# Optimization experiments

Hardware: AMD Instinct MI355X
Metric: run time of the kernel (lower is better)

Reference implementation:

```python
import jax, jax.numpy as jnp
import numpy as np

OUT, IN, GS = 16384, 4096, 16
G = OUT * IN // GS  # 4194304 groups


def setup_inputs() -> dict:
    key = jax.random.key(0)
    k1, k2, k3, k4 = jax.random.split(key, 4)
    x = jax.random.normal(k1, (8, 32, IN), dtype=jnp.float32)
    weight_q2 = jax.random.randint(k2, (G, GS // 4), 0, 256, dtype=jnp.int32)
    weight_norm = jax.random.uniform(k3, (G, 1), dtype=jnp.float16)
    bias = jax.random.normal(k4, (OUT,), dtype=jnp.float32)
    return {"x": x, "weight_q2": weight_q2, "weight_norm": weight_norm, "bias": bias}


def _dequant_2bit(weight_q2, weight_norm):
    # torch: xq_out[:, i::4] = (xq >> 2i) & 3  =>  element index within group = i + 4*k
    # where k = packed column (slow, stride 4), i = shift index (fast).
    norm = weight_norm.astype(jnp.float32)                      # [G, 1]
    shifts = jnp.arange(4, dtype=jnp.int32) * 2                 # [4]
    vals = (weight_q2[:, :, None] >> shifts) & 3                # [G, 4(pack k), 4(shift i)]
    xq_out = vals.astype(jnp.float32).reshape(G, GS)            # [G, 16], layout k*4 + i
    w = (xq_out / 3.0) * (2.0 * norm) - norm                    # [G, 16]
    return w.reshape(OUT, IN)


def reference(x, weight_q2, weight_norm, bias):
    w = _dequant_2bit(weight_q2, weight_norm)                   # [OUT, IN] fp32
    return jnp.einsum('bsi,oi->bso', x, w) + bias
```

## Files before the change

kernel.cpp:

```cpp
#include <hip/hip_runtime.h>
#include <stdint.h>

#define M_DIM 256
#define N_DIM 16384
#define K_DIM 4096
#define BN 64
#define BK 64
#define NT (K_DIM / BK)

typedef __bf16 bf16x8 __attribute__((ext_vector_type(8)));
typedef float  f32x4  __attribute__((ext_vector_type(4)));

__device__ __forceinline__ uint32_t f2bf(float f) {
  uint32_t u = __float_as_uint(f);
  return (u + 0x7fffu + ((u >> 16) & 1u)) >> 16;
}

#define LDS_BARRIER() \
  asm volatile("s_waitcnt lgkmcnt(0)\n\ts_barrier" ::: "memory")

__global__ __launch_bounds__(256) void cvt_x_kernel(const float* __restrict__ x,
                                                    uint4* __restrict__ ws) {
  int T = blockIdx.x * 256 + threadIdx.x;
  int mb_glob = T >> 13;
  int r       = T & 8191;
  int kch     = r >> 6;
  int L       = r & 63;
  int row = mb_glob * 16 + (L & 15);
  int k   = kch * 32 + (L >> 4) * 8;
  const float* p = x + (size_t)row * K_DIM + k;
  float4 a = *(const float4*)p;
  float4 b = *(const float4*)(p + 4);
  uint4 o;
  o.x = f2bf(a.x) | (f2bf(a.y) << 16);
  o.y = f2bf(a.z) | (f2bf(a.w) << 16);
  o.z = f2bf(b.x) | (f2bf(b.y) << 16);
  o.w = f2bf(b.z) | (f2bf(b.w) << 16);
  ws[T] = o;
}

__device__ __forceinline__ uint4 deq8(uint32_t qx, uint32_t qy, uint32_t tlo,
                                      uint32_t thi) {
  uint32_t s0 = ((qx & 3u) | ((qx & 0xCu) << 14)) * 0x0202u + 0x01000100u;
  uint32_t s1 = (((qx >> 4) & 3u) | ((qx & 0xC0u) << 10)) * 0x0202u + 0x01000100u;
  uint32_t s2 = ((qy & 3u) | ((qy & 0xCu) << 14)) * 0x0202u + 0x01000100u;
  uint32_t s3 = (((qy >> 4) & 3u) | ((qy & 0xC0u) << 10)) * 0x0202u + 0x01000100u;
  uint4 r;
  r.x = __builtin_amdgcn_perm(thi, tlo, s0);
  r.y = __builtin_amdgcn_perm(thi, tlo, s1);
  r.z = __builtin_amdgcn_perm(thi, tlo, s2);
  r.w = __builtin_amdgcn_perm(thi, tlo, s3);
  return r;
}

__global__ __launch_bounds__(512, 4) void gemm2bit_kernel(
    const uint4*    __restrict__ aws,
    const uint32_t* __restrict__ q2,
    const float*    __restrict__ nrm,
    const float*    __restrict__ bias,
    float*          __restrict__ out)
{
  __shared__ uint4 Bb[2][512];

  const int tid  = threadIdx.x;
  const int lane = tid & 63;
  const int w    = tid >> 6;
  const int lo4  = lane & 15;
  const int qd   = lane >> 4;
  const int n0   = blockIdx.x * BN;
  const int m0   = blockIdx.y * 128;

  if (w < 4) {
    const int cw  = w;
    const int lrs = lane ^ qd;

    const uint4* pA = aws + (size_t)(blockIdx.y * 8 + cw * 2) * 8192 + lane;

    f32x4 acc[2][4];
#pragma unroll
    for (int s = 0; s < 2; ++s)
#pragma unroll
      for (int u = 0; u < 4; ++u)
        acc[s][u] = (f32x4){0.f, 0.f, 0.f, 0.f};

    uint4 afE[4], afO[4];
#pragma unroll
    for (int s = 0; s < 2; ++s)
#pragma unroll
      for (int ts = 0; ts < 2; ++ts)
        afE[s * 2 + ts] = pA[(size_t)s * 8192 + ts * 64];
    LDS_BARRIER();

#define CONS_BODY(T, PR, AFC, AFN)                                              \
    do {                                                                        \
      if ((T) + 1 < NT) {                                                       \
        size_t toff = (size_t)((T) + 1) * 128;                                  \
        _Pragma("unroll")                                                       \
        for (int s = 0; s < 2; ++s)                                             \
          _Pragma("unroll")                                                     \
          for (int ts = 0; ts < 2; ++ts)                                        \
            AFN[s * 2 + ts] = pA[(size_t)s * 8192 + toff + ts * 64];            \
      }                                                                         \
      __builtin_amdgcn_s_setprio(1);                                            \
      _Pragma("unroll")                                                         \
      for (int ts = 0; ts < 2; ++ts) {                                          \
        bf16x8 bfv[4];                                                          \
        _Pragma("unroll")                                                       \
        for (int u = 0; u < 4; ++u)                                             \
          bfv[u] = *(const bf16x8*)&Bb[PR][(ts * 4 + u) * 64 + lrs];            \
        _Pragma("unroll")                                                       \
        for (int s = 0; s < 2; ++s) {                                           \
          bf16x8 av = __builtin_bit_cast(bf16x8, AFC[s * 2 + ts]);              \
          _Pragma("unroll")                                                     \
          for (int u = 0; u < 4; ++u)                                           \
            acc[s][u] = __builtin_amdgcn_mfma_f32_16x16x32_bf16(av, bfv[u],     \
                                                            acc[s][u], 0, 0, 0);\
        }                                                                       \
      }                                                                         \
      __builtin_amdgcn_s_setprio(0);                                            \
      LDS_BARRIER();                                                            \
    } while (0)

    for (int t2 = 0; t2 < NT; t2 += 2) {
      CONS_BODY(t2,     0, afE, afO);
      CONS_BODY(t2 + 1, 1, afO, afE);
    }
#undef CONS_BODY

    float bv[4];
#pragma unroll
    for (int u = 0; u < 4; ++u)
      bv[u] = bias[n0 + u * 16 + lo4];
#pragma unroll
    for (int s = 0; s < 2; ++s) {
      int mrow = m0 + cw * 32 + s * 16 + qd * 4;
#pragma unroll
      for (int u = 0; u < 4; ++u) {
        int ncol = n0 + u * 16 + lo4;
        float* p = out + (size_t)mrow * N_DIM + ncol;
#pragma unroll
        for (int r = 0; r < 4; ++r)
          p[(size_t)r * N_DIM] = acc[s][u][r] + bv[u];
      }
    }
  } else {
    const int pw    = w - 4;
    const int kg    = lane & 3;
    const int n_loc = lane >> 2;
    const int grow  = n0 + pw * 16 + n_loc;
    const int qd2a  = (kg & 1) * 2;
    const int qd2b  = qd2a + 1;
    const int bsA = ((kg >> 1) * 4 + pw) * 64 + qd2a * 16 + (n_loc ^ qd2a);
    const int bsB = ((kg >> 1) * 4 + pw) * 64 + qd2b * 16 + (n_loc ^ qd2b);

    const uint32_t* pq = q2 + ((size_t)grow * 256 + kg) * 4;
    const float*    pn = nrm + (size_t)grow * 256 + kg;

    uint4 q0 = *(const uint4*)pq;
    float y0 = pn[0];
    uint4 qE = *(const uint4*)(pq + 16);
    float nE = pn[4];
    uint4 qO = *(const uint4*)(pq + 32);
    float nO = pn[8];
    {
      float a2 = y0 * (2.0f / 3.0f);
      uint32_t tlo = f2bf(-y0) | (f2bf(fmaf(1.0f, a2, -y0)) << 16);
      uint32_t thi = f2bf(fmaf(2.0f, a2, -y0)) | (f2bf(fmaf(3.0f, a2, -y0)) << 16);
      Bb[0][bsA] = deq8(q0.x, q0.y, tlo, thi);
      Bb[0][bsB] = deq8(q0.z, q0.w, tlo, thi);
    }
    LDS_BARRIER();

#define PROD_BODY(T, PR, QQ, NN)                                                \
    do {                                                                        \
      if ((T) + 1 < NT) {                                                       \
        float a2 = NN * (2.0f / 3.0f);                                          \
        uint32_t tlo = f2bf(-NN) | (f2bf(fmaf(1.0f, a2, -NN)) << 16);           \
        uint32_t thi = f2bf(fmaf(2.0f, a2, -NN)) |                              \
                       (f2bf(fmaf(3.0f, a2, -NN)) << 16);                       \
        Bb[(PR) ^ 1][bsA] = deq8(QQ.x, QQ.y, tlo, thi);                         \
        Bb[(PR) ^ 1][bsB] = deq8(QQ.z, QQ.w, tlo, thi);                         \
      }                                                                         \
      if ((T) + 3 < NT) {                                                       \
        QQ = *(const uint4*)(pq + (size_t)((T) + 3) * 16);                      \
        NN = pn[(size_t)((T) + 3) * 4];                                         \
      }                                                                         \
      LDS_BARRIER();                                                            \
    } while (0)

    for (int t2 = 0; t2 < NT; t2 += 2) {
      PROD_BODY(t2,     0, qE, nE);
      PROD_BODY(t2 + 1, 1, qO, nO);
    }
#undef PROD_BODY
  }
}

extern "C" void kernel_launch(void* const* d_in, const int* in_sizes, int n_in,
                              void* d_out, int out_size, void* d_ws, size_t ws_size,
                              hipStream_t stream) {
  const float*    x    = (const float*)d_in[0];
  const uint32_t* q2   = (const uint32_t*)d_in[1];
  const float*    nm   = (const float*)d_in[2];
  const float*    bias = (const float*)d_in[3];
  float*          out  = (float*)d_out;
  uint4*          aws  = (uint4*)d_ws;

  cvt_x_kernel<<<512, 256, 0, stream>>>(x, aws);
  gemm2bit_kernel<<<dim3(N_DIM / BN, 2), 512, 0, stream>>>(aws, q2, nm, bias, out);
}
```

Baseline: 153.9 us.

## Deepen LDS ring to four stages and retile consumer warps 2x2

The shared B buffer grows from two to four stages, so producer warps dequantize two K-tiles per barrier and the barrier count is halved. Consumer warps are remapped from a 4x1 to a 2x2 layout, each computing 64 rows by 32 columns. Each consumer now reads two B fragments from LDS per step instead of four, and keeps four A fragments in flight. The cost is twice the LDS footprint and more A registers per warp, which may reduce occupancy.

```diff
diff --git a/kernel.cpp b/kernel.cpp
--- a/kernel.cpp
+++ b/kernel.cpp
@@ -60,7 +60,7 @@
     const float*    __restrict__ bias,
     float*          __restrict__ out)
 {
-  __shared__ uint4 Bb[2][512];
+  __shared__ uint4 Bb[4][512];
 
   const int tid  = threadIdx.x;
   const int lane = tid & 63;
@@ -71,72 +71,71 @@
   const int m0   = blockIdx.y * 128;
 
   if (w < 4) {
-    const int cw  = w;
+    const int wm  = w >> 1;
+    const int wn  = w & 1;
     const int lrs = lane ^ qd;
 
-    const uint4* pA = aws + (size_t)(blockIdx.y * 8 + cw * 2) * 8192 + lane;
-
-    f32x4 acc[2][4];
-#pragma unroll
-    for (int s = 0; s < 2; ++s)
-#pragma unroll
-      for (int u = 0; u < 4; ++u)
+    const uint4* pA = aws + (size_t)(blockIdx.y * 8 + wm * 4) * 8192 + lane;
+
+    f32x4 acc[4][2];
+#pragma unroll
+    for (int s = 0; s < 4; ++s)
+#pragma unroll
+      for (int u = 0; u < 2; ++u)
         acc[s][u] = (f32x4){0.f, 0.f, 0.f, 0.f};
 
     uint4 afE[4], afO[4];
 #pragma unroll
-    for (int s = 0; s < 2; ++s)
-#pragma unroll
-      for (int ts = 0; ts < 2; ++ts)
-        afE[s * 2 + ts] = pA[(size_t)s * 8192 + ts * 64];
+    for (int s = 0; s < 4; ++s) afE[s] = pA[(size_t)s * 8192];
+    const uint4* pAp = pA + 64;
+    int cnext = 1;
     LDS_BARRIER();
 
-#define CONS_BODY(T, PR, AFC, AFN)                                              \
+#define CONS_STEP(BUF, TS, AFC, AFN)                                            \
     do {                                                                        \
-      if ((T) + 1 < NT) {                                                       \
-        size_t toff = (size_t)((T) + 1) * 128;                                  \
+      if (cnext < 128) {                                                        \
         _Pragma("unroll")                                                       \
-        for (int s = 0; s < 2; ++s)                                             \
-          _Pragma("unroll")                                                     \
-          for (int ts = 0; ts < 2; ++ts)                                        \
-            AFN[s * 2 + ts] = pA[(size_t)s * 8192 + toff + ts * 64];            \
+        for (int s = 0; s < 4; ++s) AFN[s] = pAp[(size_t)s * 8192];             \
       }                                                                         \
+      pAp += 64; ++cnext;                                                       \
       __builtin_amdgcn_s_setprio(1);                                            \
+      bf16x8 bv0 = *(const bf16x8*)&Bb[BUF][((TS) * 4 + wn * 2) * 64 + lrs];    \
+      bf16x8 bv1 = *(const bf16x8*)&Bb[BUF][((TS) * 4 + wn * 2 + 1) * 64 + lrs];\
       _Pragma("unroll")                                                         \
-      for (int ts = 0; ts < 2; ++ts) {                                          \
-        bf16x8 bfv[4];                                                          \
-        _Pragma("unroll")                                                       \
-        for (int u = 0; u < 4; ++u)                                             \
-          bfv[u] = *(const bf16x8*)&Bb[PR][(ts * 4 + u) * 64 + lrs];            \
-        _Pragma("unroll")                                                       \
-        for (int s = 0; s < 2; ++s) {                                           \
-          bf16x8 av = __builtin_bit_cast(bf16x8, AFC[s * 2 + ts]);              \
-          _Pragma("unroll")                                                     \
-          for (int u = 0; u < 4; ++u)                                           \
-            acc[s][u] = __builtin_amdgcn_mfma_f32_16x16x32_bf16(av, bfv[u],     \
-                                                            acc[s][u], 0, 0, 0);\
-        }                                                                       \
+      for (int s = 0; s < 4; ++s) {                                             \
+        bf16x8 av = __builtin_bit_cast(bf16x8, AFC[s]);                         \
+        acc[s][0] = __builtin_amdgcn_mfma_f32_16x16x32_bf16(av, bv0,            \
+                                                            acc[s][0], 0, 0, 0);\
+        acc[s][1] = __builtin_amdgcn_mfma_f32_16x16x32_bf16(av, bv1,            \
+                                                            acc[s][1], 0, 0, 0);\
       }                                                                         \
       __builtin_amdgcn_s_setprio(0);                                            \
-      LDS_BARRIER();                                                            \
     } while (0)
 
-    for (int t2 = 0; t2 < NT; t2 += 2) {
-      CONS_BODY(t2,     0, afE, afO);
-      CONS_BODY(t2 + 1, 1, afO, afE);
-    }
-#undef CONS_BODY
-
-    float bv[4];
-#pragma unroll
-    for (int u = 0; u < 4; ++u)
-      bv[u] = bias[n0 + u * 16 + lo4];
-#pragma unroll
-    for (int s = 0; s < 2; ++s) {
-      int mrow = m0 + cw * 32 + s * 16 + qd * 4;
-#pragma unroll
-      for (int u = 0; u < 4; ++u) {
-        int ncol = n0 + u * 16 + lo4;
+    for (int tp = 0; tp < NT; tp += 4) {
+      CONS_STEP(0, 0, afE, afO);
+      CONS_STEP(0, 1, afO, afE);
+      CONS_STEP(1, 0, afE, afO);
+      CONS_STEP(1, 1, afO, afE);
+      LDS_BARRIER();
+      CONS_STEP(2, 0, afE, afO);
+      CONS_STEP(2, 1, afO, afE);
+      CONS_STEP(3, 0, afE, afO);
+      CONS_STEP(3, 1, afO, afE);
+      LDS_BARRIER();
+    }
+#undef CONS_STEP
+
+    float bv[2];
+#pragma unroll
+    for (int u = 0; u < 2; ++u)
+      bv[u] = bias[n0 + wn * 32 + u * 16 + lo4];
+#pragma unroll
+    for (int s = 0; s < 4; ++s) {
+      int mrow = m0 + wm * 64 + s * 16 + qd * 4;
+#pragma unroll
+      for (int u = 0; u < 2; ++u) {
+        int ncol = n0 + wn * 32 + u * 16 + lo4;
         float* p = out + (size_t)mrow * N_DIM + ncol;
 #pragma unroll
         for (int r = 0; r < 4; ++r)
@@ -156,43 +155,53 @@
     const uint32_t* pq = q2 + ((size_t)grow * 256 + kg) * 4;
     const float*    pn = nrm + (size_t)grow * 256 + kg;
 
-    uint4 q0 = *(const uint4*)pq;
-    float y0 = pn[0];
-    uint4 qE = *(const uint4*)(pq + 16);
-    float nE = pn[4];
-    uint4 qO = *(const uint4*)(pq + 32);
-    float nO = pn[8];
+#define DEQ_TILE(WB, Q, NV)                                                     \
+    do {                                                                        \
+      float a2_ = (NV) * (2.0f / 3.0f);                                         \
+      uint32_t tlo_ = f2bf(-(NV)) | (f2bf(fmaf(1.0f, a2_, -(NV))) << 16);       \
+      uint32_t thi_ = f2bf(fmaf(2.0f, a2_, -(NV))) |                            \
+                      (f2bf(fmaf(3.0f, a2_, -(NV))) << 16);                     \
+      Bb[WB][bsA] = deq8((Q).x, (Q).y, tlo_, thi_);                             \
+      Bb[WB][bsB] = deq8((Q).z, (Q).w, tlo_, thi_);                             \
+    } while (0)
+
     {
-      float a2 = y0 * (2.0f / 3.0f);
-      uint32_t tlo = f2bf(-y0) | (f2bf(fmaf(1.0f, a2, -y0)) << 16);
-      uint32_t thi = f2bf(fmaf(2.0f, a2, -y0)) | (f2bf(fmaf(3.0f, a2, -y0)) << 16);
-      Bb[0][bsA] = deq8(q0.x, q0.y, tlo, thi);
-      Bb[0][bsB] = deq8(q0.z, q0.w, tlo, thi);
-    }
+      uint4 t0 = *(const uint4*)pq;         float y0 = pn[0];
+      uint4 t1 = *(const uint4*)(pq + 16);  float y1 = pn[4];
+      DEQ_TILE(0, t0, y0);
+      DEQ_TILE(1, t1, y1);
+    }
+    uint4 qE0 = *(const uint4*)(pq + 32);  float nE0 = pn[8];
+    uint4 qE1 = *(const uint4*)(pq + 48);  float nE1 = pn[12];
+    uint4 qO0 = *(const uint4*)(pq + 64);  float nO0 = pn[16];
+    uint4 qO1 = *(const uint4*)(pq + 80);  float nO1 = pn[20];
+    const uint32_t* pql = pq + 96;
+    const float*    pnl = pn + 24;
     LDS_BARRIER();
 
-#define PROD_BODY(T, PR, QQ, NN)                                                \
-    do {                                                                        \
-      if ((T) + 1 < NT) {                                                       \
-        float a2 = NN * (2.0f / 3.0f);                                          \
-        uint32_t tlo = f2bf(-NN) | (f2bf(fmaf(1.0f, a2, -NN)) << 16);           \
-        uint32_t thi = f2bf(fmaf(2.0f, a2, -NN)) |                              \
-                       (f2bf(fmaf(3.0f, a2, -NN)) << 16);                       \
-        Bb[(PR) ^ 1][bsA] = deq8(QQ.x, QQ.y, tlo, thi);                         \
-        Bb[(PR) ^ 1][bsB] = deq8(QQ.z, QQ.w, tlo, thi);                         \
-      }                                                                         \
-      if ((T) + 3 < NT) {                                                       \
-        QQ = *(const uint4*)(pq + (size_t)((T) + 3) * 16);                      \
-        NN = pn[(size_t)((T) + 3) * 4];                                         \
-      }                                                                         \
-      LDS_BARRIER();                                                            \
-    } while (0)
-
-    for (int t2 = 0; t2 < NT; t2 += 2) {
-      PROD_BODY(t2,     0, qE, nE);
-      PROD_BODY(t2 + 1, 1, qO, nO);
-    }
-#undef PROD_BODY
+    for (int tp = 0; tp < NT; tp += 4) {
+      if (tp + 2 < NT) {
+        DEQ_TILE(2, qE0, nE0);
+        DEQ_TILE(3, qE1, nE1);
+      }
+      if (tp + 6 < NT) {
+        qE0 = *(const uint4*)pql;        nE0 = pnl[0];
+        qE1 = *(const uint4*)(pql + 16); nE1 = pnl[4];
+      }
+      pql += 32; pnl += 8;
+      LDS_BARRIER();
+      if (tp + 4 < NT) {
+        DEQ_TILE(0, qO0, nO0);
+        DEQ_TILE(1, qO1, nO1);
+      }
+      if (tp + 8 < NT) {
+        qO0 = *(const uint4*)pql;        nO0 = pnl[0];
+        qO1 = *(const uint4*)(pql + 16); nO1 = pnl[4];
+      }
+      pql += 32; pnl += 8;
+      LDS_BARRIER();
+    }
+#undef DEQ_TILE
   }
 }
 
```

Result: slower. 161.1 us (+4.7%).

## Halve block M-tile to 64 rows with two consumer and two producer waves

Applied to the files above, without the earlier changes.

Shrinks each workgroup from 512 to 256 threads: two consumer waves cover 64 M rows and two producer waves each dequantize two weight rows per step. The grid doubles in the M dimension to 4 to keep coverage the same. This gives finer scheduling granularity and more blocks per CU, but the full weight matrix is now loaded and dequantized four times instead of twice, which doubles the producer-side global traffic and ALU work.

```diff
diff --git a/kernel.cpp b/kernel.cpp
--- a/kernel.cpp
+++ b/kernel.cpp
@@ -53,7 +53,7 @@
   return r;
 }
 
-__global__ __launch_bounds__(512, 4) void gemm2bit_kernel(
+__global__ __launch_bounds__(256) void gemm2bit_kernel(
     const uint4*    __restrict__ aws,
     const uint32_t* __restrict__ q2,
     const float*    __restrict__ nrm,
@@ -68,13 +68,13 @@
   const int lo4  = lane & 15;
   const int qd   = lane >> 4;
   const int n0   = blockIdx.x * BN;
-  const int m0   = blockIdx.y * 128;
-
-  if (w < 4) {
+  const int m0   = blockIdx.y * 64;
+
+  if (w < 2) {
     const int cw  = w;
     const int lrs = lane ^ qd;
 
-    const uint4* pA = aws + (size_t)(blockIdx.y * 8 + cw * 2) * 8192 + lane;
+    const uint4* pA = aws + (size_t)(blockIdx.y * 4 + cw * 2) * 8192 + lane;
 
     f32x4 acc[2][4];
 #pragma unroll
@@ -144,55 +144,70 @@
       }
     }
   } else {
-    const int pw    = w - 4;
+    const int p     = w - 2;
     const int kg    = lane & 3;
     const int n_loc = lane >> 2;
-    const int grow  = n0 + pw * 16 + n_loc;
+    const int ra    = n0 + p * 32 + n_loc;
+    const int rb    = ra + 16;
+    const int nba   = p * 2;
+    const int nbb   = p * 2 + 1;
     const int qd2a  = (kg & 1) * 2;
     const int qd2b  = qd2a + 1;
-    const int bsA = ((kg >> 1) * 4 + pw) * 64 + qd2a * 16 + (n_loc ^ qd2a);
-    const int bsB = ((kg >> 1) * 4 + pw) * 64 + qd2b * 16 + (n_loc ^ qd2b);
-
-    const uint32_t* pq = q2 + ((size_t)grow * 256 + kg) * 4;
-    const float*    pn = nrm + (size_t)grow * 256 + kg;
-
-    uint4 q0 = *(const uint4*)pq;
-    float y0 = pn[0];
-    uint4 qE = *(const uint4*)(pq + 16);
-    float nE = pn[4];
-    uint4 qO = *(const uint4*)(pq + 32);
-    float nO = pn[8];
+    const int ba    = ((kg >> 1) * 4 + nba) * 64;
+    const int bb    = ((kg >> 1) * 4 + nbb) * 64;
+    const int sAa = ba + qd2a * 16 + (n_loc ^ qd2a);
+    const int sBa = ba + qd2b * 16 + (n_loc ^ qd2b);
+    const int sAb = bb + qd2a * 16 + (n_loc ^ qd2a);
+    const int sBb = bb + qd2b * 16 + (n_loc ^ qd2b);
+
+    const uint32_t* pqa = q2 + ((size_t)ra * 256 + kg) * 4;
+    const uint32_t* pqb = q2 + ((size_t)rb * 256 + kg) * 4;
+    const float*    pna = nrm + (size_t)ra * 256 + kg;
+    const float*    pnb = nrm + (size_t)rb * 256 + kg;
+
+#define DEQ_GROUP(WB, Q, NV, SA, SB)                                            \
+    do {                                                                        \
+      float a2_ = (NV) * (2.0f / 3.0f);                                         \
+      uint32_t tlo_ = f2bf(-(NV)) | (f2bf(fmaf(1.0f, a2_, -(NV))) << 16);       \
+      uint32_t thi_ = f2bf(fmaf(2.0f, a2_, -(NV))) |                            \
+                      (f2bf(fmaf(3.0f, a2_, -(NV))) << 16);                     \
+      Bb[WB][SA] = deq8((Q).x, (Q).y, tlo_, thi_);                              \
+      Bb[WB][SB] = deq8((Q).z, (Q).w, tlo_, thi_);                              \
+    } while (0)
+
     {
-      float a2 = y0 * (2.0f / 3.0f);
-      uint32_t tlo = f2bf(-y0) | (f2bf(fmaf(1.0f, a2, -y0)) << 16);
-      uint32_t thi = f2bf(fmaf(2.0f, a2, -y0)) | (f2bf(fmaf(3.0f, a2, -y0)) << 16);
-      Bb[0][bsA] = deq8(q0.x, q0.y, tlo, thi);
-      Bb[0][bsB] = deq8(q0.z, q0.w, tlo, thi);
-    }
+      uint4 t0a = *(const uint4*)pqa;  float y0a = pna[0];
+      uint4 t0b = *(const uint4*)pqb;  float y0b = pnb[0];
+      DEQ_GROUP(0, t0a, y0a, sAa, sBa);
+      DEQ_GROUP(0, t0b, y0b, sAb, sBb);
+    }
+    uint4 qEa = *(const uint4*)(pqa + 16);  float nEa = pna[4];
+    uint4 qEb = *(const uint4*)(pqb + 16);  float nEb = pnb[4];
+    uint4 qOa = *(const uint4*)(pqa + 32);  float nOa = pna[8];
+    uint4 qOb = *(const uint4*)(pqb + 32);  float nOb = pnb[8];
     LDS_BARRIER();
 
-#define PROD_BODY(T, PR, QQ, NN)                                                \
+#define PROD_BODY(T, PR, QA, NA, QB, NB)                                        \
     do {                                                                        \
       if ((T) + 1 < NT) {                                                       \
-        float a2 = NN * (2.0f / 3.0f);                                          \
-        uint32_t tlo = f2bf(-NN) | (f2bf(fmaf(1.0f, a2, -NN)) << 16);           \
-        uint32_t thi = f2bf(fmaf(2.0f, a2, -NN)) |                              \
-                       (f2bf(fmaf(3.0f, a2, -NN)) << 16);                       \
-        Bb[(PR) ^ 1][bsA] = deq8(QQ.x, QQ.y, tlo, thi);                         \
-        Bb[(PR) ^ 1][bsB] = deq8(QQ.z, QQ.w, tlo, thi);                         \
+        DEQ_GROUP((PR) ^ 1, QA, NA, sAa, sBa);                                  \
+        DEQ_GROUP((PR) ^ 1, QB, NB, sAb, sBb);                                  \
       }                                                                         \
       if ((T) + 3 < NT) {                                                       \
-        QQ = *(const uint4*)(pq + (size_t)((T) + 3) * 16);                      \
-        NN = pn[(size_t)((T) + 3) * 4];                                         \
+        QA = *(const uint4*)(pqa + (size_t)((T) + 3) * 16);                     \
+        NA = pna[(size_t)((T) + 3) * 4];                                        \
+        QB = *(const uint4*)(pqb + (size_t)((T) + 3) * 16);                     \
+        NB = pnb[(size_t)((T) + 3) * 4];                                        \
       }                                                                         \
       LDS_BARRIER();                                                            \
     } while (0)
 
     for (int t2 = 0; t2 < NT; t2 += 2) {
-      PROD_BODY(t2,     0, qE, nE);
-      PROD_BODY(t2 + 1, 1, qO, nO);
+      PROD_BODY(t2,     0, qEa, nEa, qEb, nEb);
+      PROD_BODY(t2 + 1, 1, qOa, nOa, qOb, nOb);
     }
 #undef PROD_BODY
+#undef DEQ_GROUP
   }
 }
 
@@ -207,5 +222,5 @@
   uint4*          aws  = (uint4*)d_ws;
 
   cvt_x_kernel<<<512, 256, 0, stream>>>(x, aws);
-  gemm2bit_kernel<<<dim3(N_DIM / BN, 2), 512, 0, stream>>>(aws, q2, nm, bias, out);
-}
+  gemm2bit_kernel<<<dim3(N_DIM / BN, 4), 256, 0, stream>>>(aws, q2, nm, bias, out);
+}
```

After: 167.9 us. 1.09x slower.
